# Performance work log

Hardware: AMD Instinct MI355X
Metric: run time of the kernel (lower is better)

Reference implementation:

```python
import jax, jax.numpy as jnp
import numpy as np

TOP_K = 2

def setup_inputs() -> dict:
    key = jax.random.key(0)
    k1, k2 = jax.random.split(key)
    N, D, E = 16384, 2048, 64
    x = jax.random.normal(k1, (N, D), dtype=jnp.float32)
    W = jax.random.normal(k2, (D, E), dtype=jnp.float32) * (1.0 / np.sqrt(D))
    b = jnp.zeros((E,), dtype=jnp.float32)
    return {"x": x, "W": W, "b": b}

def reference(x, W, b):
    # gate linear: [N, D] @ [D, E] + [E]
    logits = jnp.einsum('nd,de->ne', x, W) + b
    gates = jax.nn.softmax(logits, axis=-1)
    topk_vals, topk_idx = jax.lax.top_k(gates, TOP_K)  # [N, k]
    N = gates.shape[0]
    rows = jnp.arange(N)[:, None]  # [N, 1] broadcast over k
    dispatch_mask = jnp.zeros_like(gates).at[rows, topk_idx].set(topk_vals)
    return dispatch_mask, topk_idx
```

## Files before the change

### kernel.cpp

```cpp
#include <hip/hip_runtime.h>
#include <math.h>

#define NROWS 16384
#define DDIM  2048
#define EEXP  64
#define RB    32
#define NST   8
#define CHSTRIDE 24576

typedef short        bf16x8 __attribute__((ext_vector_type(8)));
typedef float        f32x16 __attribute__((ext_vector_type(16)));
typedef float        f32x4  __attribute__((ext_vector_type(4)));
typedef unsigned int u32x4  __attribute__((ext_vector_type(4)));

union V4 { u32x4 u; bf16x8 s; };

static __device__ __forceinline__ void split3x2(float f0, float f1,
                                                unsigned int &p0, unsigned int &p1,
                                                unsigned int &p2) {
    unsigned int a0 = __float_as_uint(f0), b0 = __float_as_uint(f1);
    unsigned int ah = a0 & 0xffff0000u,   bh = b0 & 0xffff0000u;
    float fa1 = f0 - __uint_as_float(ah);
    float fb1 = f1 - __uint_as_float(bh);
    unsigned int a1 = __float_as_uint(fa1), b1 = __float_as_uint(fb1);
    unsigned int am = a1 & 0xffff0000u,     bm = b1 & 0xffff0000u;
    float fa2 = fa1 - __uint_as_float(am);
    float fb2 = fb1 - __uint_as_float(bm);
    p0 = (a0 >> 16) | bh;
    p1 = (a1 >> 16) | bm;
    p2 = (__float_as_uint(fa2) >> 16) | (__float_as_uint(fb2) & 0xffff0000u);
}

static __device__ __forceinline__ void cvt8(f32x4 u, f32x4 v, V4 &q0, V4 &q1, V4 &q2) {
    unsigned int a, b, c;
    split3x2(u[0], u[1], a, b, c); q0.u[0] = a; q1.u[0] = b; q2.u[0] = c;
    split3x2(u[2], u[3], a, b, c); q0.u[1] = a; q1.u[1] = b; q2.u[1] = c;
    split3x2(v[0], v[1], a, b, c); q0.u[2] = a; q1.u[2] = b; q2.u[2] = c;
    split3x2(v[2], v[3], a, b, c); q0.u[3] = a; q1.u[3] = b; q2.u[3] = c;
}

#define MM(ACC, A, B) ACC = __builtin_amdgcn_mfma_f32_32x32x16_bf16((A), (B), ACC, 0, 0, 0)

__global__ __launch_bounds__(256)
void wsplit_kernel(const float* __restrict__ W, unsigned char* __restrict__ ws) {
    const int t  = blockIdx.x * 256 + threadIdx.x;
    const int e  = t & 63;
    const int ko = t >> 6;
    const int k0 = ko * 8;
    f32x4 u, v;
#pragma unroll
    for (int j = 0; j < 4; ++j) u[j] = W[(size_t)(k0 + j) * EEXP + e];
#pragma unroll
    for (int j = 0; j < 4; ++j) v[j] = W[(size_t)(k0 + 4 + j) * EEXP + e];
    V4 q0, q1, q2;
    cvt8(u, v, q0, q1, q2);
    const int c  = ko >> 3;
    const int kg = (ko >> 1) & 3;
    const int h  = ko & 1;
    const int et = e >> 5;
    const int ln = h * 32 + (e & 31);
    unsigned char* d = ws + (size_t)((c * 8 + kg * 2 + et) * 3) * 1024 + ln * 16;
    *(u32x4*)(d +    0) = q0.u;
    *(u32x4*)(d + 1024) = q1.u;
    *(u32x4*)(d + 2048) = q2.u;
}

__global__ __launch_bounds__(512, 2)
void router_kernel(const float* __restrict__ x,
                   const unsigned char* __restrict__ wsplit,
                   const float* __restrict__ bias_v,
                   float* __restrict__ mask_out,
                   float* __restrict__ idx_out) {
    __shared__ __align__(16) float smem[16384];

    const int tid  = threadIdx.x;
    const int lane = tid & 63;
    const int w    = __builtin_amdgcn_readfirstlane(tid >> 6);
    const int kg   = w & 3;
    const int et   = w >> 2;
    const int l31  = lane & 31;
    const int h    = lane >> 5;

    const int bid  = blockIdx.x;
    const int bswz = (bid & 7) * ((int)gridDim.x >> 3) + (bid >> 3);
    const int row0 = bswz * RB;

    const int srow = 4 * w;

#define GLL(I, BAND, BUF)                                                     \
    __builtin_amdgcn_global_load_lds(                                         \
        (const __attribute__((address_space(1))) void*)                       \
            (x + (size_t)(row0 + srow + (I)) * DDIM + (BAND)                  \
               + ((lane ^ ((srow + (I)) & 7)) << 2)),                         \
        (__attribute__((address_space(3))) void*)                             \
            (smem + (BUF) * 8192 + (srow + (I)) * 256),                       \
        16, 0, 0);

    const unsigned char* wq = wsplit + (size_t)((kg * 2 + et) * 3) * 1024 + lane * 16;

    f32x16 accA, accB;
#pragma unroll
    for (int i = 0; i < 16; ++i) { accA[i] = 0.f; accB[i] = 0.f; }

    GLL(0, 0, 0) GLL(1, 0, 0) GLL(2, 0, 0) GLL(3, 0, 0)
    __syncthreads();

#pragma unroll 1
    for (int s = 0; s < NST; ++s) {
        const int buf = s & 1;

        if (s + 1 < NST) {
            const int band = (s + 1) * 256;
            const int nb = buf ^ 1;
            GLL(0, band, nb) GLL(1, band, nb) GLL(2, band, nb) GLL(3, band, nb)
        }

        const float* xb = smem + buf * 8192 + l31 * 256;
        const int xr = l31 & 7;
#pragma unroll
        for (int cc = 0; cc < 4; ++cc) {
            const int k0 = cc * 64 + kg * 16 + h * 8;
            const int bb = k0 >> 2;
            f32x4 lo = *(const f32x4*)(xb + (((bb    ) ^ xr) << 2));
            f32x4 hi = *(const f32x4*)(xb + (((bb + 1) ^ xr) << 2));
            const unsigned char* q = wq + (size_t)(s * 4 + cc) * CHSTRIDE;
            V4 b0, b1, b2;
            b0.u = *(const u32x4*)(q);
            b1.u = *(const u32x4*)(q + 1024);
            b2.u = *(const u32x4*)(q + 2048);
            V4 a0, a1, a2;
            cvt8(lo, hi, a0, a1, a2);
            MM(accA, a0.s, b0.s); MM(accB, a0.s, b1.s); MM(accA, a1.s, b0.s);
            MM(accB, a0.s, b2.s); MM(accA, a1.s, b1.s); MM(accB, a2.s, b0.s);
        }

        __syncthreads();
    }

    float* ep = smem;
#pragma unroll
    for (int r = 0; r < 16; ++r) {
        const int rowl = (r & 3) + 8 * (r >> 2) + 4 * h;
        ep[kg * 2048 + rowl * 64 + et * 32 + l31] = accA[r] + accB[r];
    }
    __syncthreads();

    const float bias = bias_v[lane];
#pragma unroll
    for (int rr = 0; rr < 4; ++rr) {
        const int rl  = w * 4 + rr;
        const int row = row0 + rl;
        float logit = bias + ep[rl * 64 + lane]
                           + ep[2048 + rl * 64 + lane]
                           + ep[4096 + rl * 64 + lane]
                           + ep[6144 + rl * 64 + lane];

        float m = logit;
#pragma unroll
        for (int off = 32; off >= 1; off >>= 1) m = fmaxf(m, __shfl_xor(m, off));
        float ex = __expf(logit - m);
        float s = ex;
#pragma unroll
        for (int off = 32; off >= 1; off >>= 1) s += __shfl_xor(s, off);
        float gate = ex / s;

        float v1 = logit; int i1 = lane;
#pragma unroll
        for (int off = 32; off >= 1; off >>= 1) {
            float ov = __shfl_xor(v1, off);
            int   oi = __shfl_xor(i1, off);
            if (ov > v1 || (ov == v1 && oi < i1)) { v1 = ov; i1 = oi; }
        }
        float v2 = (lane == i1) ? -INFINITY : logit; int i2 = lane;
#pragma unroll
        for (int off = 32; off >= 1; off >>= 1) {
            float ov = __shfl_xor(v2, off);
            int   oi = __shfl_xor(i2, off);
            if (ov > v2 || (ov == v2 && oi < i2)) { v2 = ov; i2 = oi; }
        }

        float outv = (lane == i1 || lane == i2) ? gate : 0.0f;
        mask_out[(size_t)row * EEXP + lane] = outv;
        if (lane == 0) {
            idx_out[row * 2 + 0] = (float)i1;
            idx_out[row * 2 + 1] = (float)i2;
        }
    }
}

extern "C" void kernel_launch(void* const* d_in, const int* in_sizes, int n_in,
                              void* d_out, int out_size, void* d_ws, size_t ws_size,
                              hipStream_t stream) {
    const float* x = (const float*)d_in[0];
    const float* W = (const float*)d_in[1];
    const float* b = (const float*)d_in[2];
    float* mask_out = (float*)d_out;
    float* idx_out  = mask_out + (size_t)NROWS * EEXP;
    unsigned char* ws = (unsigned char*)d_ws;

    wsplit_kernel<<<dim3(64), dim3(256), 0, stream>>>(W, ws);
    router_kernel<<<dim3(NROWS / RB), dim3(512), 0, stream>>>(x, ws, b, mask_out, idx_out);
}
```

Measured before the change: 207.8 us.

## Split K dimension across four blocks and add separate finish kernel

```diff
diff --git a/kernel.cpp b/kernel.cpp
--- a/kernel.cpp
+++ b/kernel.cpp
@@ -5,8 +5,10 @@
 #define DDIM  2048
 #define EEXP  64
 #define RB    32
-#define NST   8
+#define KSPLIT 4
+#define CHB    8
 #define CHSTRIDE 24576
+#define PART_OFF (1u << 20)
 
 typedef short        bf16x8 __attribute__((ext_vector_type(8)));
 typedef float        f32x16 __attribute__((ext_vector_type(16)));
@@ -65,13 +67,11 @@
     *(u32x4*)(d + 2048) = q2.u;
 }
 
-__global__ __launch_bounds__(512, 2)
-void router_kernel(const float* __restrict__ x,
+__global__ __launch_bounds__(512, 3)
+void matmul_kernel(const float* __restrict__ x,
                    const unsigned char* __restrict__ wsplit,
-                   const float* __restrict__ bias_v,
-                   float* __restrict__ mask_out,
-                   float* __restrict__ idx_out) {
-    __shared__ __align__(16) float smem[16384];
+                   float* __restrict__ part) {
+    __shared__ __align__(16) float smem[8192];
 
     const int tid  = threadIdx.x;
     const int lane = tid & 63;
@@ -83,77 +83,94 @@
 
     const int bid  = blockIdx.x;
     const int bswz = (bid & 7) * ((int)gridDim.x >> 3) + (bid >> 3);
-    const int row0 = bswz * RB;
-
-    const int srow = 4 * w;
-
-#define GLL(I, BAND, BUF)                                                     \
+    const int rg   = bswz >> 2;
+    const int ks   = bswz & 3;
+    const int row0 = rg * RB;
+    const int c0   = ks * CHB;
+
+    const int strow = tid >> 4;
+    const int sslot = (tid & 15) ^ (strow & 7);
+    const float* xsrc = x + (size_t)(row0 + strow) * DDIM + c0 * 64 + sslot * 4;
+    float* sdst = smem + strow * 64 + (tid & 15) * 4;
+
+#define GLL(S, BUF)                                                           \
     __builtin_amdgcn_global_load_lds(                                         \
-        (const __attribute__((address_space(1))) void*)                       \
-            (x + (size_t)(row0 + srow + (I)) * DDIM + (BAND)                  \
-               + ((lane ^ ((srow + (I)) & 7)) << 2)),                         \
-        (__attribute__((address_space(3))) void*)                             \
-            (smem + (BUF) * 8192 + (srow + (I)) * 256),                       \
+        (const __attribute__((address_space(1))) void*)(xsrc + (S) * 64),     \
+        (__attribute__((address_space(3))) void*)(sdst + (BUF) * 4096),       \
         16, 0, 0);
 
-    const unsigned char* wq = wsplit + (size_t)((kg * 2 + et) * 3) * 1024 + lane * 16;
+    const unsigned char* wq = wsplit + (size_t)((kg * 2 + et) * 3) * 1024
+                            + lane * 16 + (size_t)c0 * CHSTRIDE;
+
+    const int bb = kg * 4 + h * 2;
+    const int xr = l31 & 7;
+    const int loOff = l31 * 64 + (((bb    ) ^ xr) << 2);
+    const int hiOff = l31 * 64 + (((bb + 1) ^ xr) << 2);
 
     f32x16 accA, accB;
 #pragma unroll
     for (int i = 0; i < 16; ++i) { accA[i] = 0.f; accB[i] = 0.f; }
 
-    GLL(0, 0, 0) GLL(1, 0, 0) GLL(2, 0, 0) GLL(3, 0, 0)
+    GLL(0, 0)
     __syncthreads();
 
 #pragma unroll 1
-    for (int s = 0; s < NST; ++s) {
+    for (int s = 0; s < CHB; ++s) {
         const int buf = s & 1;
-
-        if (s + 1 < NST) {
-            const int band = (s + 1) * 256;
-            const int nb = buf ^ 1;
-            GLL(0, band, nb) GLL(1, band, nb) GLL(2, band, nb) GLL(3, band, nb)
-        }
-
-        const float* xb = smem + buf * 8192 + l31 * 256;
-        const int xr = l31 & 7;
-#pragma unroll
-        for (int cc = 0; cc < 4; ++cc) {
-            const int k0 = cc * 64 + kg * 16 + h * 8;
-            const int bb = k0 >> 2;
-            f32x4 lo = *(const f32x4*)(xb + (((bb    ) ^ xr) << 2));
-            f32x4 hi = *(const f32x4*)(xb + (((bb + 1) ^ xr) << 2));
-            const unsigned char* q = wq + (size_t)(s * 4 + cc) * CHSTRIDE;
-            V4 b0, b1, b2;
-            b0.u = *(const u32x4*)(q);
-            b1.u = *(const u32x4*)(q + 1024);
-            b2.u = *(const u32x4*)(q + 2048);
-            V4 a0, a1, a2;
-            cvt8(lo, hi, a0, a1, a2);
-            MM(accA, a0.s, b0.s); MM(accB, a0.s, b1.s); MM(accA, a1.s, b0.s);
-            MM(accB, a0.s, b2.s); MM(accA, a1.s, b1.s); MM(accB, a2.s, b0.s);
-        }
+        if (s + 1 < CHB) { GLL(s + 1, buf ^ 1) }
+
+        const float* xb = smem + buf * 4096;
+        f32x4 lo = *(const f32x4*)(xb + loOff);
+        f32x4 hi = *(const f32x4*)(xb + hiOff);
+        const unsigned char* q = wq + (size_t)s * CHSTRIDE;
+        V4 b0, b1, b2;
+        b0.u = *(const u32x4*)(q);
+        b1.u = *(const u32x4*)(q + 1024);
+        b2.u = *(const u32x4*)(q + 2048);
+        V4 a0, a1, a2;
+        cvt8(lo, hi, a0, a1, a2);
+        MM(accA, a0.s, b0.s); MM(accB, a0.s, b1.s); MM(accA, a1.s, b0.s);
+        MM(accB, a0.s, b2.s); MM(accA, a1.s, b1.s); MM(accB, a2.s, b0.s);
 
         __syncthreads();
     }
 
-    float* ep = smem;
 #pragma unroll
     for (int r = 0; r < 16; ++r) {
         const int rowl = (r & 3) + 8 * (r >> 2) + 4 * h;
-        ep[kg * 2048 + rowl * 64 + et * 32 + l31] = accA[r] + accB[r];
+        smem[kg * 2048 + rowl * 64 + et * 32 + l31] = accA[r] + accB[r];
     }
     __syncthreads();
-
+    f32x4 s0 = *(const f32x4*)(smem + tid * 4);
+    f32x4 s1 = *(const f32x4*)(smem + 2048 + tid * 4);
+    f32x4 s2 = *(const f32x4*)(smem + 4096 + tid * 4);
+    f32x4 s3 = *(const f32x4*)(smem + 6144 + tid * 4);
+    f32x4 t;
+#pragma unroll
+    for (int i = 0; i < 4; ++i) t[i] = s0[i] + s1[i] + s2[i] + s3[i];
+    *(f32x4*)(part + (size_t)(rg * 4 + ks) * 2048 + tid * 4) = t;
+}
+
+__global__ __launch_bounds__(512)
+void finish_kernel(const float* __restrict__ part,
+                   const float* __restrict__ bias_v,
+                   float* __restrict__ mask_out,
+                   float* __restrict__ idx_out) {
+    const int tid  = threadIdx.x;
+    const int lane = tid & 63;
+    const int w    = __builtin_amdgcn_readfirstlane(tid >> 6);
+    const int b    = blockIdx.x;
     const float bias = bias_v[lane];
+    const float* p0 = part + (size_t)b * 4 * 2048;
+
 #pragma unroll
     for (int rr = 0; rr < 4; ++rr) {
         const int rl  = w * 4 + rr;
-        const int row = row0 + rl;
-        float logit = bias + ep[rl * 64 + lane]
-                           + ep[2048 + rl * 64 + lane]
-                           + ep[4096 + rl * 64 + lane]
-                           + ep[6144 + rl * 64 + lane];
+        const int row = b * 32 + rl;
+        float logit = bias + p0[rl * 64 + lane]
+                           + p0[2048 + rl * 64 + lane]
+                           + p0[4096 + rl * 64 + lane]
+                           + p0[6144 + rl * 64 + lane];
 
         float m = logit;
 #pragma unroll
@@ -197,7 +214,9 @@
     float* mask_out = (float*)d_out;
     float* idx_out  = mask_out + (size_t)NROWS * EEXP;
     unsigned char* ws = (unsigned char*)d_ws;
+    float* part = (float*)(ws + PART_OFF);
 
     wsplit_kernel<<<dim3(64), dim3(256), 0, stream>>>(W, ws);
-    router_kernel<<<dim3(NROWS / RB), dim3(512), 0, stream>>>(x, ws, b, mask_out, idx_out);
-}
+    matmul_kernel<<<dim3((NROWS / RB) * KSPLIT), dim3(512), 0, stream>>>(x, ws, part);
+    finish_kernel<<<dim3(NROWS / RB), dim3(512), 0, stream>>>(part, b, mask_out, idx_out);
+}
```

After: 218.4 us. +5.1%, slower.
